# Kernel tuning notes

Hardware: AMD Instinct MI355X
Metric: run time of the kernel (lower is better)

Reference implementation:

```python
import jax, jax.numpy as jnp
import numpy as np

HID = 256
HEADS = 8
DPH = HID // HEADS  # 32
N = 65536
E = 262144


def _ln(x, g, b):
    m = jnp.mean(x, axis=-1, keepdims=True)
    v = jnp.var(x, axis=-1, keepdims=True)
    return (x - m) * jax.lax.rsqrt(v + 1e-5) * g + b


def _gelu(x):
    return jax.nn.gelu(x, approximate=False)


def _mlp2(x, W1, b1, W2, b2, act):
    return act(x @ W1 + b1) @ W2 + b2


def setup_inputs() -> dict:
    key = jax.random.key(0)
    ks = jax.random.split(key, 32)
    d = {}
    d["x"] = jax.random.normal(ks[0], (N, HID), jnp.float32)
    d["edge_index"] = jax.random.randint(ks[1], (2, E), 0, N, dtype=jnp.int32)
    d["edge_attr"] = jax.random.normal(ks[2], (E, 7), jnp.float32)
    i = 3
    def p(shape, s=0.02):
        nonlocal i
        out = jax.random.normal(ks[i], shape, jnp.float32) * s
        i += 1
        return out
    for nm, (din, dh, do) in [("q", (2 * HID + 3, 2 * HID, HID)),
                              ("k", (2 * HID + 3, 2 * HID, HID)),
                              ("v", (2 * HID + 3, 2 * HID, HID)),
                              ("s", (4, 64, HEADS)),
                              ("f", (HID, 2 * HID, HID))]:
        d[nm + "W1"] = p((din, dh))
        d[nm + "b1"] = jnp.zeros((dh,), jnp.float32)
        d[nm + "W2"] = p((dh, do))
        d[nm + "b2"] = jnp.zeros((do,), jnp.float32)
    d["ln_g"] = jnp.ones((HID,), jnp.float32)
    d["ln_b"] = jnp.zeros((HID,), jnp.float32)
    d["rW"] = p((2 * HID, HID))
    d["rb"] = jnp.zeros((HID,), jnp.float32)
    return d


def reference(x, edge_index, edge_attr,
              qW1, qb1, qW2, qb2,
              kW1, kb1, kW2, kb2,
              vW1, vb1, vW2, vb2,
              sW1, sb1, sW2, sb2,
              ln_g, ln_b, rW, rb,
              fW1, fb1, fW2, fb2):
    n_nodes = x.shape[0]
    original_x = x
    residual = x
    xn = _ln(x, ln_g, ln_b)

    src = edge_index[0]
    dst = edge_index[1]
    # gather endpoint features, concat with molecular edge feats -> [E, 2*HID+3]
    comb = jnp.concatenate([xn[src], xn[dst], edge_attr[:, :3]], axis=1)

    Q = _mlp2(comb, qW1, qb1, qW2, qb2, _gelu).reshape(-1, HEADS, DPH)
    K = _mlp2(comb, kW1, kb1, kW2, kb2, _gelu).reshape(-1, HEADS, DPH)
    V = _mlp2(comb, vW1, vb1, vW2, vb2, _gelu).reshape(-1, HEADS, DPH)

    scale = jnp.sqrt(jnp.float32(DPH))
    scores = jnp.einsum('ehd,egd->ehg', Q, K) / scale  # [E, H, H]
    bias = _mlp2(edge_attr[:, 3:7], sW1, sb1, sW2, sb2, jax.nn.relu)[:, :, None]  # [E, H, 1]
    attn = jax.nn.softmax(scores + bias, axis=1)  # softmax over dim=1, as in torch code
    wv = jnp.einsum('ehg,egd->ehd', attn, V).reshape(-1, HID)  # [E, HID]

    # scatter-mean to target nodes (edge_index[1])
    sums = jax.ops.segment_sum(wv, dst, num_segments=n_nodes)
    cnt = jax.ops.segment_sum(jnp.ones((wv.shape[0],), wv.dtype), dst, num_segments=n_nodes)
    out = sums / jnp.maximum(cnt, 1.0)[:, None]

    x1 = residual + out
    fused = jnp.concatenate([x1, original_x], axis=-1)
    x2 = x1 + (fused @ rW + rb)
    x3 = x2 + _mlp2(_ln(x2, ln_g, ln_b), fW1, fb1, fW2, fb2, _gelu)
    return x3
```

## Files before the change

### kernel.cpp

```cpp
#include <hip/hip_runtime.h>

#define N_NODES 65536
#define N_EDGES 262144
#define EBATCH 32768

typedef unsigned short u16;
typedef unsigned char u8;
typedef float f32x4 __attribute__((ext_vector_type(4)));
typedef _Float16 h2 __attribute__((ext_vector_type(2)));
typedef _Float16 v8h __attribute__((ext_vector_type(8)));

__device__ __forceinline__ u16 f2h(float f) {
  return __builtin_bit_cast(u16, (_Float16)f);
}
__device__ __forceinline__ u8 f2e5m2(float f) {
  _Float16 h = (_Float16)f;
  u16 hb = __builtin_bit_cast(u16, h);
  hb = (u16)(hb + 0x7F + ((hb >> 8) & 1));
  return (u8)(hb >> 8);
}
__device__ __forceinline__ void dec4(unsigned d, float* o) {
  o[0] = (float)__builtin_bit_cast(_Float16, (u16)((d << 8) & 0xFF00u));
  o[1] = (float)__builtin_bit_cast(_Float16, (u16)(d & 0xFF00u));
  o[2] = (float)__builtin_bit_cast(_Float16, (u16)((d >> 8) & 0xFF00u));
  o[3] = (float)__builtin_bit_cast(_Float16, (u16)((d >> 16) & 0xFF00u));
}
__device__ __forceinline__ h2 e5lo(unsigned d) {
  return __builtin_bit_cast(h2, __builtin_amdgcn_perm(d, 0u, 0x05000400u));
}
__device__ __forceinline__ h2 e5hi(unsigned d) {
  return __builtin_bit_cast(h2, __builtin_amdgcn_perm(d, 0u, 0x07000600u));
}
__device__ __forceinline__ float gelu_s(float x) {
  float e = __expf(1.702f * x);
  return x - __fdividef(x, e + 1.0f);
}
__device__ __forceinline__ float gelu_f(float x) {
  float y = 1.5957691216057308f * (x + 0.044715f * x * x * x);
  float e = __expf(y);
  return x - __fdividef(x, e + 1.0f);
}
__device__ __forceinline__ void gld16(const u16* g, u16* l) {
  __builtin_amdgcn_global_load_lds(
      (const __attribute__((address_space(1))) void*)g,
      (__attribute__((address_space(3))) void*)l, 16, 0, 0);
}

__global__ __launch_bounds__(256) void ln_kernel(const float* __restrict__ x,
                                                 const float* __restrict__ g,
                                                 const float* __restrict__ b,
                                                 u16* __restrict__ out) {
  int row = blockIdx.x * 4 + (threadIdx.x >> 6);
  int lane = threadIdx.x & 63;
  float4 v = ((const float4*)(x + (size_t)row * 256))[lane];
  float s = v.x + v.y + v.z + v.w;
  float s2 = v.x * v.x + v.y * v.y + v.z * v.z + v.w * v.w;
#pragma unroll
  for (int off = 1; off < 64; off <<= 1) {
    s += __shfl_xor(s, off, 64);
    s2 += __shfl_xor(s2, off, 64);
  }
  float mean = s * (1.0f / 256.0f);
  float var = s2 * (1.0f / 256.0f) - mean * mean;
  float rs = rsqrtf(var + 1e-5f);
  float4 gv = ((const float4*)g)[lane];
  float4 bv = ((const float4*)b)[lane];
  ushort4 o;
  o.x = f2h((v.x - mean) * rs * gv.x + bv.x);
  o.y = f2h((v.y - mean) * rs * gv.y + bv.y);
  o.z = f2h((v.z - mean) * rs * gv.z + bv.z);
  o.w = f2h((v.w - mean) * rs * gv.w + bv.w);
  *(ushort4*)(out + (size_t)row * 256 + lane * 4) = o;
}

#define GEMM_CORE(K_)                                                                   \
  const int t = threadIdx.x;                                                            \
  const int wave = t >> 6, lane = t & 63;                                               \
  const int lrow = lane & 15, quad = lane >> 4;                                         \
  const int wrow = (wave & 1) * 64, wcol = (wave >> 1) * 64;                            \
  const int sa0 = 2 * wave, sa1 = 2 * wave + 1;                                         \
  const u16* pa0 = A + (size_t)(tm + sa0 * 16 + lrow) * (K_) + quad * 8;                \
  const u16* pa1 = A + (size_t)(tm + sa1 * 16 + lrow) * (K_) + quad * 8;                \
  const u16* pb0 = BT + (size_t)(tn + sa0 * 16 + lrow) * (K_) + quad * 8;               \
  const u16* pb1 = BT + (size_t)(tn + sa1 * 16 + lrow) * (K_) + quad * 8;               \
  u16* la0 = &sAB[sa0 * 512];                                                           \
  u16* la1 = &sAB[sa1 * 512];                                                           \
  u16* lb0 = &sAB[4096 + sa0 * 512];                                                    \
  u16* lb1 = &sAB[4096 + sa1 * 512];                                                    \
  f32x4 acc[4][4];                                                                      \
  {                                                                                     \
    const f32x4 z = {0.f, 0.f, 0.f, 0.f};                                               \
    _Pragma("unroll") for (int i = 0; i < 4; ++i)                                       \
        _Pragma("unroll") for (int j = 0; j < 4; ++j) acc[i][j] = z;                    \
  }                                                                                     \
  for (int k0 = 0; k0 < (K_); k0 += 32) {                                               \
    gld16(pa0, la0);                                                                    \
    gld16(pa1, la1);                                                                    \
    gld16(pb0, lb0);                                                                    \
    gld16(pb1, lb1);                                                                    \
    pa0 += 32;                                                                          \
    pa1 += 32;                                                                          \
    pb0 += 32;                                                                          \
    pb1 += 32;                                                                          \
    __syncthreads();                                                                    \
    v8h af[4], bfv[4];                                                                  \
    _Pragma("unroll") for (int i = 0; i < 4; ++i) af[i] =                               \
        *(const v8h*)&sAB[((wave & 1) * 4 + i) * 512 + lane * 8];                       \
    _Pragma("unroll") for (int j = 0; j < 4; ++j) bfv[j] =                              \
        *(const v8h*)&sAB[4096 + ((wave >> 1) * 4 + j) * 512 + lane * 8];               \
    _Pragma("unroll") for (int i = 0; i < 4; ++i)                                       \
        _Pragma("unroll") for (int j = 0; j < 4; ++j) acc[i][j] =                       \
            __builtin_amdgcn_mfma_f32_16x16x32_f16(af[i], bfv[j], acc[i][j], 0, 0, 0);  \
    __syncthreads();                                                                    \
  }

template <typename Epi>
__global__ __launch_bounds__(256) void gemm2(const u16* __restrict__ A,
                                             const u16* __restrict__ BT,
                                             int K, int NT, Epi epi) {
  __shared__ __align__(16) u16 sAB[8192];
  const int bid = blockIdx.x;
  const int mt = bid / NT, nt = bid % NT;
  const int tm = mt * 128, tn = nt * 128;
  GEMM_CORE(K)
#pragma unroll
  for (int i = 0; i < 4; ++i)
#pragma unroll
    for (int j = 0; j < 4; ++j)
#pragma unroll
      for (int rg = 0; rg < 4; ++rg)
        epi(tm + wrow + i * 16 + quad * 4 + rg, tn + wcol + j * 16 + lrow, acc[i][j][rg]);
}

__global__ __launch_bounds__(256) void gemm2_ab(const u16* __restrict__ A,
                                                const u16* __restrict__ BT,
                                                const float* __restrict__ b1cat,
                                                u8* __restrict__ out) {
  __shared__ __align__(16) u16 sAB[8192];
  const int bid = blockIdx.x;
  const int local = bid >> 3;
  const int mt = (bid & 7) * 64 + local / 24;
  const int nt = local % 24;
  const int tm = mt * 128, tn = nt * 128;
  GEMM_CORE(256)
  float bj[4];
#pragma unroll
  for (int j = 0; j < 4; ++j)
    bj[j] = (nt < 12) ? b1cat[tn + wcol + j * 16 + lrow] : 0.f;
  u8* sb = (u8*)sAB;
#pragma unroll
  for (int i = 0; i < 4; ++i)
#pragma unroll
    for (int j = 0; j < 4; ++j)
#pragma unroll
      for (int rg = 0; rg < 4; ++rg)
        sb[(wrow + i * 16 + quad * 4 + rg) * 128 + wcol + j * 16 + lrow] =
            f2e5m2(acc[i][j][rg] + bj[j]);
  __syncthreads();
  {
    int r = t >> 1, half = t & 1;
    const uint4* sp = (const uint4*)&sb[r * 128 + half * 64];
    uint4* dp = (uint4*)(out + (size_t)(tm + r) * 3072 + tn + half * 64);
    dp[0] = sp[0];
    dp[1] = sp[1];
    dp[2] = sp[2];
    dp[3] = sp[3];
  }
}

struct EpiX2 {
  float* x2;
  const float* x1;
  const float* rb;
  __device__ void operator()(int m, int n, float v) const {
    x2[(size_t)m * 256 + n] = v + rb[n] + x1[(size_t)m * 256 + n];
  }
};
struct EpiHf {
  u16* hf;
  const float* b1;
  __device__ void operator()(int m, int n, float v) const {
    hf[(size_t)m * 512 + n] = f2h(gelu_f(v + b1[n]));
  }
};
struct EpiOut {
  float* out;
  const float* b2;
  const float* x2;
  __device__ void operator()(int m, int n, float v) const {
    out[(size_t)m * 256 + n] = v + b2[n] + x2[(size_t)m * 256 + n];
  }
};

__global__ void prep_w1catT(u16* __restrict__ out, const float* __restrict__ qW1,
                            const float* __restrict__ kW1, const float* __restrict__ vW1) {
  int cIdx = blockIdx.x;
  int rIdx = threadIdx.x;
  int sec = cIdx >> 9;
  int h = cIdx & 511;
  int mlp = sec % 3;
  const float* W1 = (mlp == 0) ? qW1 : (mlp == 1) ? kW1 : vW1;
  int rowoff = (sec < 3) ? 0 : 256;
  out[(size_t)cIdx * 256 + rIdx] = f2h(W1[(size_t)(rowoff + rIdx) * 512 + h]);
}
__global__ void prep_w2T(u16* __restrict__ out, const float* __restrict__ qW2,
                         const float* __restrict__ kW2, const float* __restrict__ vW2) {
  int row = blockIdx.x;
  int m = row >> 8, n = row & 255;
  const float* W2 = (m == 0) ? qW2 : (m == 1) ? kW2 : vW2;
  for (int k = threadIdx.x; k < 512; k += 256)
    out[(size_t)row * 512 + k] = f2h(W2[(size_t)k * 256 + n]);
}
__global__ void transpose_cast(u16* __restrict__ out, const float* __restrict__ in, int K, int Nn) {
  int n = blockIdx.x;
  for (int k = threadIdx.x; k < K; k += blockDim.x)
    out[(size_t)n * K + k] = f2h(in[(size_t)k * Nn + n]);
}
__global__ void prep_w1e16(u16* __restrict__ out, const float* __restrict__ qW1,
                           const float* __restrict__ kW1, const float* __restrict__ vW1) {
  int b = blockIdx.x;
  int m = b / 3, r = b % 3;
  const float* W1 = (m == 0) ? qW1 : (m == 1) ? kW1 : vW1;
  out[(size_t)b * 512 + threadIdx.x] = f2h(W1[(size_t)(512 + r) * 512 + threadIdx.x]);
}
__global__ void prep_b1cat(float* __restrict__ out, const float* __restrict__ qb1,
                           const float* __restrict__ kb1, const float* __restrict__ vb1) {
  int idx = blockIdx.x * 256 + threadIdx.x;
  const float* b = (idx < 512) ? qb1 : (idx < 1024) ? kb1 : vb1;
  out[idx] = b[idx & 511];
}

__global__ __launch_bounds__(256) void hist_kernel(const int* __restrict__ dst,
                                                   unsigned* __restrict__ cnt) {
  int e = blockIdx.x * 256 + threadIdx.x;
  atomicAdd(&cnt[dst[e]], 1u);
}
__global__ __launch_bounds__(1024) void scan_kernel(const unsigned* __restrict__ cnt,
                                                    unsigned* __restrict__ off,
                                                    unsigned* __restrict__ woff) {
  __shared__ unsigned s_part[1024];
  int t = threadIdx.x;
  unsigned local[64];
  unsigned run = 0;
  const uint4* cp = (const uint4*)(cnt + t * 64);
#pragma unroll
  for (int j = 0; j < 16; ++j) {
    uint4 v = cp[j];
    local[j * 4 + 0] = v.x; local[j * 4 + 1] = v.y;
    local[j * 4 + 2] = v.z; local[j * 4 + 3] = v.w;
  }
#pragma unroll
  for (int j = 0; j < 64; ++j) { unsigned c = local[j]; local[j] = run; run += c; }
  s_part[t] = run;
  __syncthreads();
  for (int d = 1; d < 1024; d <<= 1) {
    unsigned v = (t >= d) ? s_part[t - d] : 0u;
    __syncthreads();
    s_part[t] += v;
    __syncthreads();
  }
  unsigned base = (t == 0) ? 0u : s_part[t - 1];
  for (int j = 0; j < 64; ++j) {
    unsigned o = base + local[j];
    off[t * 64 + j] = o;
    woff[t * 64 + j] = o;
  }
}
__global__ __launch_bounds__(256) void scatter_ids(const int* __restrict__ dst,
                                                   unsigned* __restrict__ woff,
                                                   unsigned* __restrict__ eid) {
  int e = blockIdx.x * 256 + threadIdx.x;
  unsigned pos = atomicAdd(&woff[dst[e]], 1u);
  eid[pos] = (unsigned)e;
}

__global__ __launch_bounds__(256) void qkv_gemm(
    const int* __restrict__ eidx, const float* __restrict__ eattr,
    const u8* __restrict__ AB, const u16* __restrict__ W2T, const u16* __restrict__ w1e16,
    const float* __restrict__ qb2, const float* __restrict__ kb2, const float* __restrict__ vb2,
    int ebase, u8* __restrict__ qkv) {
  __shared__ __align__(16) u16 sH[64][136];
  __shared__ int s_src[64], s_dst[64];
  __shared__ __align__(16) float s_ea[64][4];
  const int m = blockIdx.y;
  const int t = threadIdx.x;
  const int e0 = ebase + blockIdx.x * 64;
  if (t < 64) {
    s_src[t] = eidx[e0 + t];
    s_dst[t] = eidx[N_EDGES + e0 + t];
  } else if (t >= 128 && t < 192) {
    int i = t - 128;
    const float* ea = eattr + (size_t)(e0 + i) * 7;
    s_ea[i][0] = ea[0]; s_ea[i][1] = ea[1]; s_ea[i][2] = ea[2];
  }
  __syncthreads();
  const int i = t & 63, seg = t >> 6;
  const int lane = t & 63, wave = t >> 6;
  const int lrow = lane & 15, quad = lane >> 4;
  const int wrow = (wave & 1) * 32, wcol = (wave >> 1) * 128;
  h2 ea0h, ea1h, ea2h;
  ea0h[0] = ea0h[1] = (_Float16)s_ea[i][0];
  ea1h[0] = ea1h[1] = (_Float16)s_ea[i][1];
  ea2h[0] = ea2h[1] = (_Float16)s_ea[i][2];
  const u8* rsB = AB + (size_t)s_src[i] * 3072 + m * 512 + seg * 32;
  const u8* rdB = AB + (size_t)s_dst[i] * 3072 + 1536 + m * 512 + seg * 32;
  const unsigned* w32 = (const unsigned*)(w1e16 + (size_t)m * 1536);
  f32x4 acc[2][8];
  const f32x4 z = {0.f, 0.f, 0.f, 0.f};
#pragma unroll
  for (int i2 = 0; i2 < 2; ++i2)
#pragma unroll
    for (int j = 0; j < 8; ++j) acc[i2][j] = z;
  for (int k0 = 0; k0 < 512; k0 += 128) {
    {
      alignas(16) unsigned sd[8], dd[8];
      *(uint4*)&sd[0] = *(const uint4*)(rsB + k0);
      *(uint4*)&sd[4] = *(const uint4*)(rsB + k0 + 16);
      *(uint4*)&dd[0] = *(const uint4*)(rdB + k0);
      *(uint4*)&dd[4] = *(const uint4*)(rdB + k0 + 16);
      const int cp0 = (k0 + seg * 32) >> 1;
      alignas(16) unsigned hout[16];
#pragma unroll
      for (int d = 0; d < 8; ++d) {
        int cp = cp0 + d * 2;
        h2 slo = e5lo(sd[d]) + e5lo(dd[d]);
        h2 shi = e5hi(sd[d]) + e5hi(dd[d]);
        slo += ea0h * __builtin_bit_cast(h2, w32[cp]);
        shi += ea0h * __builtin_bit_cast(h2, w32[cp + 1]);
        slo += ea1h * __builtin_bit_cast(h2, w32[256 + cp]);
        shi += ea1h * __builtin_bit_cast(h2, w32[256 + cp + 1]);
        slo += ea2h * __builtin_bit_cast(h2, w32[512 + cp]);
        shi += ea2h * __builtin_bit_cast(h2, w32[512 + cp + 1]);
        float g0 = gelu_s((float)slo[0]), g1 = gelu_s((float)slo[1]);
        float g2 = gelu_s((float)shi[0]), g3 = gelu_s((float)shi[1]);
        hout[d * 2] = (unsigned)f2h(g0) | ((unsigned)f2h(g1) << 16);
        hout[d * 2 + 1] = (unsigned)f2h(g2) | ((unsigned)f2h(g3) << 16);
      }
      uint4* hp = (uint4*)&sH[i][seg * 32];
      hp[0] = *(const uint4*)&hout[0];
      hp[1] = *(const uint4*)&hout[4];
      hp[2] = *(const uint4*)&hout[8];
      hp[3] = *(const uint4*)&hout[12];
    }
    __syncthreads();
#pragma unroll
    for (int ks = 0; ks < 4; ++ks) {
      int kk = ks * 32;
      v8h a0 = *(const v8h*)&sH[wrow + lrow][kk + quad * 8];
      v8h a1 = *(const v8h*)&sH[wrow + 16 + lrow][kk + quad * 8];
#pragma unroll
      for (int j = 0; j < 8; ++j) {
        v8h b = *(const v8h*)&W2T[(size_t)(m * 256 + wcol + j * 16 + lrow) * 512 + k0 + kk + quad * 8];
        acc[0][j] = __builtin_amdgcn_mfma_f32_16x16x32_f16(a0, b, acc[0][j], 0, 0, 0);
        acc[1][j] = __builtin_amdgcn_mfma_f32_16x16x32_f16(a1, b, acc[1][j], 0, 0, 0);
      }
    }
    __syncthreads();
  }
  const float* b2 = (m == 0) ? qb2 : (m == 1) ? kb2 : vb2;
  u8* sb = (u8*)sH;
#pragma unroll
  for (int i2 = 0; i2 < 2; ++i2)
#pragma unroll
    for (int j = 0; j < 8; ++j)
#pragma unroll
      for (int rg = 0; rg < 4; ++rg) {
        int row = wrow + i2 * 16 + quad * 4 + rg;
        int col = wcol + j * 16 + lrow;
        sb[row * 272 + col] = f2e5m2(acc[i2][j][rg] + b2[col]);
      }
  __syncthreads();
  {
    int ir = t >> 2, sg = t & 3;
    const u8* srcp = &sb[ir * 272 + sg * 64];
    uint4* dstp = (uint4*)(qkv + (size_t)(blockIdx.x * 64 + ir) * 768 + m * 256 + sg * 64);
    dstp[0] = *(const uint4*)srcp;
    dstp[1] = *(const uint4*)(srcp + 16);
    dstp[2] = *(const uint4*)(srcp + 32);
    dstp[3] = *(const uint4*)(srcp + 48);
  }
}

__global__ __launch_bounds__(256) void attn_kernel(
    const u8* __restrict__ qkv, const float* __restrict__ eattr,
    const float* __restrict__ sW1, const float* __restrict__ sb1,
    const float* __restrict__ sW2, const float* __restrict__ sb2,
    int ebase, u8* __restrict__ wv) {
  __shared__ __align__(16) u8 sQ[32][784];
  __shared__ float sS[32][8][8];
  const int t = threadIdx.x;
  const int el0 = blockIdx.x * 32;
  const int i = t >> 3, h = t & 7;
  {
    const uint4* g = (const uint4*)(qkv + (size_t)(el0 + i) * 768);
    uint4* l = (uint4*)&sQ[i][0];
#pragma unroll
    for (int j = 0; j < 6; ++j) l[h + j * 8] = g[h + j * 8];
  }
  float bias;
  {
    const float* ea = eattr + (size_t)(ebase + el0 + i) * 7;
    float a0 = ea[3], a1 = ea[4], a2 = ea[5], a3 = ea[6];
    float acc = sb2[h];
#pragma unroll 4
    for (int j = 0; j < 64; ++j) {
      float zz = fmaxf(a0 * sW1[j] + a1 * sW1[64 + j] + a2 * sW1[128 + j] + a3 * sW1[192 + j] + sb1[j], 0.f);
      acc += zz * sW2[j * 8 + h];
    }
    bias = acc;
  }
  __syncthreads();
  {
    alignas(16) unsigned qd[8];
    *(uint4*)&qd[0] = *(const uint4*)&sQ[i][h * 32];
    *(uint4*)&qd[4] = *(const uint4*)&sQ[i][h * 32 + 16];
    h2 qh[16];
#pragma unroll
    for (int d = 0; d < 8; ++d) { qh[d * 2] = e5lo(qd[d]); qh[d * 2 + 1] = e5hi(qd[d]); }
    float sc[8];
#pragma unroll
    for (int g = 0; g < 8; ++g) {
      alignas(16) unsigned kd[8];
      *(uint4*)&kd[0] = *(const uint4*)&sQ[i][256 + g * 32];
      *(uint4*)&kd[4] = *(const uint4*)&sQ[i][256 + g * 32 + 16];
      h2 acc;
      acc[0] = acc[1] = (_Float16)0.f;
#pragma unroll
      for (int d = 0; d < 8; ++d) {
        acc += qh[d * 2] * e5lo(kd[d]);
        acc += qh[d * 2 + 1] * e5hi(kd[d]);
      }
      sc[g] = (float)acc[0] + (float)acc[1];
    }
#pragma unroll
    for (int g = 0; g < 8; ++g) sS[i][h][g] = sc[g] * 0.17677669529663687f + bias;
  }
  __syncthreads();
  {
    int g = h;
    float mx = -1e30f;
#pragma unroll
    for (int hh = 0; hh < 8; ++hh) mx = fmaxf(mx, sS[i][hh][g]);
    float ev[8], ssum = 0.f;
#pragma unroll
    for (int hh = 0; hh < 8; ++hh) {
      ev[hh] = __expf(sS[i][hh][g] - mx);
      ssum += ev[hh];
    }
    float inv = 1.0f / ssum;
#pragma unroll
    for (int hh = 0; hh < 8; ++hh) sS[i][hh][g] = ev[hh] * inv;
  }
  __syncthreads();
  {
    h2 va[16];
#pragma unroll
    for (int u = 0; u < 16; ++u) va[u][0] = va[u][1] = (_Float16)0.f;
#pragma unroll
    for (int g = 0; g < 8; ++g) {
      float at = sS[i][h][g];
      h2 at2;
      at2[0] = at2[1] = (_Float16)at;
      alignas(16) unsigned vd[8];
      *(uint4*)&vd[0] = *(const uint4*)&sQ[i][512 + g * 32];
      *(uint4*)&vd[4] = *(const uint4*)&sQ[i][512 + g * 32 + 16];
#pragma unroll
      for (int d = 0; d < 8; ++d) {
        va[d * 2] += at2 * e5lo(vd[d]);
        va[d * 2 + 1] += at2 * e5hi(vd[d]);
      }
    }
    alignas(16) unsigned od[8];
#pragma unroll
    for (int p = 0; p < 8; ++p) {
      unsigned a = __builtin_bit_cast(unsigned, va[p * 2]) + 0x00800080u;
      unsigned b = __builtin_bit_cast(unsigned, va[p * 2 + 1]) + 0x00800080u;
      od[p] = __builtin_amdgcn_perm(b, a, 0x07050301u);
    }
    u8* dp = wv + (size_t)(ebase + el0 + i) * 256 + h * 32;
    *(uint4*)dp = *(const uint4*)&od[0];
    *(uint4*)(dp + 16) = *(const uint4*)&od[4];
  }
}

__global__ __launch_bounds__(256) void node_gather(const unsigned* __restrict__ off,
                                                   const unsigned* __restrict__ cnt,
                                                   const unsigned* __restrict__ eid,
                                                   const u8* __restrict__ wv,
                                                   const float* __restrict__ x,
                                                   float* __restrict__ x1,
                                                   u16* __restrict__ X1cat) {
  int n = blockIdx.x * 4 + (threadIdx.x >> 6);
  int lane = threadIdx.x & 63;
  unsigned st = off[n], c = cnt[n];
  float a0 = 0.f, a1 = 0.f, a2 = 0.f, a3 = 0.f;
  for (unsigned j = 0; j < c; ++j) {
    unsigned e = eid[st + j];
    unsigned d = *(const unsigned*)(wv + (size_t)e * 256 + lane * 4);
    float f[4];
    dec4(d, f);
    a0 += f[0]; a1 += f[1]; a2 += f[2]; a3 += f[3];
  }
  float inv = 1.0f / fmaxf((float)c, 1.0f);
  float4 xv = *(const float4*)(x + (size_t)n * 256 + lane * 4);
  float4 x1v = {xv.x + a0 * inv, xv.y + a1 * inv, xv.z + a2 * inv, xv.w + a3 * inv};
  *(float4*)(x1 + (size_t)n * 256 + lane * 4) = x1v;
  ushort4 a, bq;
  a.x = f2h(x1v.x); a.y = f2h(x1v.y); a.z = f2h(x1v.z); a.w = f2h(x1v.w);
  bq.x = f2h(xv.x); bq.y = f2h(xv.y); bq.z = f2h(xv.z); bq.w = f2h(xv.w);
  *(ushort4*)(X1cat + (size_t)n * 512 + lane * 4) = a;
  *(ushort4*)(X1cat + (size_t)n * 512 + 256 + lane * 4) = bq;
}

extern "C" void kernel_launch(void* const* d_in, const int* in_sizes, int n_in,
                              void* d_out, int out_size, void* d_ws, size_t ws_size,
                              hipStream_t stream) {
  const float* x = (const float*)d_in[0];
  const int* eidx = (const int*)d_in[1];
  const float* eattr = (const float*)d_in[2];
  const float* qW1 = (const float*)d_in[3];
  const float* qb1 = (const float*)d_in[4];
  const float* qW2 = (const float*)d_in[5];
  const float* qb2 = (const float*)d_in[6];
  const float* kW1 = (const float*)d_in[7];
  const float* kb1 = (const float*)d_in[8];
  const float* kW2 = (const float*)d_in[9];
  const float* kb2 = (const float*)d_in[10];
  const float* vW1 = (const float*)d_in[11];
  const float* vb1 = (const float*)d_in[12];
  const float* vW2 = (const float*)d_in[13];
  const float* vb2 = (const float*)d_in[14];
  const float* sW1 = (const float*)d_in[15];
  const float* sb1 = (const float*)d_in[16];
  const float* sW2 = (const float*)d_in[17];
  const float* sb2 = (const float*)d_in[18];
  const float* fW1 = (const float*)d_in[19];
  const float* fb1 = (const float*)d_in[20];
  const float* fW2 = (const float*)d_in[21];
  const float* fb2 = (const float*)d_in[22];
  const float* lng = (const float*)d_in[23];
  const float* lnb = (const float*)d_in[24];
  const float* rW = (const float*)d_in[25];
  const float* rb = (const float*)d_in[26];

  const size_t N = N_NODES;
  char* ws = (char*)d_ws;
  size_t off_b = 0;
  auto alloc = [&](size_t bytes) {
    void* p = ws + off_b;
    off_b = (off_b + bytes + 255) & ~(size_t)255;
    return p;
  };
  u16* W1catT = (u16*)alloc((size_t)3072 * 256 * 2);
  u16* W2T = (u16*)alloc((size_t)768 * 512 * 2);
  u16* rWT = (u16*)alloc((size_t)256 * 512 * 2);
  u16* fW1T = (u16*)alloc((size_t)512 * 256 * 2);
  u16* fW2T = (u16*)alloc((size_t)256 * 512 * 2);
  u16* w1e16 = (u16*)alloc((size_t)9 * 512 * 2);
  float* b1cat = (float*)alloc((size_t)1536 * 4);
  unsigned* cnt = (unsigned*)alloc(N * 4);
  unsigned* offs = (unsigned*)alloc(N * 4);
  unsigned* woff = (unsigned*)alloc(N * 4);
  unsigned* eid = (unsigned*)alloc((size_t)N_EDGES * 4);
  u8* qkv = (u8*)alloc((size_t)EBATCH * 768);
  u8* AB = (u8*)alloc(N * 3072);
  u16* xn = (u16*)d_out;
  u8* wv = (u8*)d_out;
  float* x1 = (float*)AB;
  u16* X1cat = (u16*)(AB + (size_t)67108864);
  float* x2 = (float*)(AB + (size_t)134217728);
  u16* xn2 = (u16*)AB;
  u16* Hf = (u16*)(AB + (size_t)33554432);

  hipMemsetAsync(cnt, 0, N * 4, stream);
  hist_kernel<<<N_EDGES / 256, 256, 0, stream>>>(eidx + N_EDGES, cnt);
  scan_kernel<<<1, 1024, 0, stream>>>(cnt, offs, woff);
  scatter_ids<<<N_EDGES / 256, 256, 0, stream>>>(eidx + N_EDGES, woff, eid);
  prep_w1catT<<<3072, 256, 0, stream>>>(W1catT, qW1, kW1, vW1);
  prep_w2T<<<768, 256, 0, stream>>>(W2T, qW2, kW2, vW2);
  prep_w1e16<<<9, 512, 0, stream>>>(w1e16, qW1, kW1, vW1);
  prep_b1cat<<<6, 256, 0, stream>>>(b1cat, qb1, kb1, vb1);
  transpose_cast<<<256, 256, 0, stream>>>(rWT, rW, 512, 256);
  transpose_cast<<<512, 256, 0, stream>>>(fW1T, fW1, 256, 512);
  transpose_cast<<<256, 256, 0, stream>>>(fW2T, fW2, 512, 256);

  ln_kernel<<<N_NODES / 4, 256, 0, stream>>>(x, lng, lnb, xn);
  gemm2_ab<<<12288, 256, 0, stream>>>(xn, W1catT, b1cat, AB);
  for (int b = 0; b < N_EDGES / EBATCH; ++b) {
    int ebase = b * EBATCH;
    qkv_gemm<<<dim3(EBATCH / 64, 3), 256, 0, stream>>>(eidx, eattr, AB, W2T, w1e16,
                                                       qb2, kb2, vb2, ebase, qkv);
    attn_kernel<<<EBATCH / 32, 256, 0, stream>>>(qkv, eattr, sW1, sb1, sW2, sb2, ebase, wv);
  }
  node_gather<<<N_NODES / 4, 256, 0, stream>>>(offs, cnt, eid, wv, x, x1, X1cat);
  gemm2<<<N_NODES / 128 * 2, 256, 0, stream>>>(X1cat, rWT, 512, 2, EpiX2{x2, x1, rb});
  ln_kernel<<<N_NODES / 4, 256, 0, stream>>>(x2, lng, lnb, xn2);
  gemm2<<<N_NODES / 128 * 4, 256, 0, stream>>>(xn2, fW1T, 256, 4, EpiHf{Hf, fb1});
  gemm2<<<N_NODES / 128 * 2, 256, 0, stream>>>(Hf, fW2T, 512, 2, EpiOut{(float*)d_out, fb2, x2});
}
```

Before: 1.980 ms.

## Double-buffer LDS tiles in GEMM core and pad fp8 epilogue staging

Replaces the single-buffered GEMM main loop with a double-buffered version that issues the next K-slice's global-to-LDS loads before computing on the current slice, cutting one barrier per iteration. K becomes a template parameter so the loop can fully unroll. The gemm2_ab epilogue pads its LDS staging rows to 136 bytes to reduce bank conflicts and copies out with 8-byte stores. LDS per block doubles to 32KB, which may lower occupancy.

```diff
diff --git a/kernel.cpp b/kernel.cpp
--- a/kernel.cpp
+++ b/kernel.cpp
@@ -73,56 +73,67 @@
   *(ushort4*)(out + (size_t)row * 256 + lane * 4) = o;
 }
 
-#define GEMM_CORE(K_)                                                                   \
-  const int t = threadIdx.x;                                                            \
-  const int wave = t >> 6, lane = t & 63;                                               \
-  const int lrow = lane & 15, quad = lane >> 4;                                         \
-  const int wrow = (wave & 1) * 64, wcol = (wave >> 1) * 64;                            \
-  const int sa0 = 2 * wave, sa1 = 2 * wave + 1;                                         \
-  const u16* pa0 = A + (size_t)(tm + sa0 * 16 + lrow) * (K_) + quad * 8;                \
-  const u16* pa1 = A + (size_t)(tm + sa1 * 16 + lrow) * (K_) + quad * 8;                \
-  const u16* pb0 = BT + (size_t)(tn + sa0 * 16 + lrow) * (K_) + quad * 8;               \
-  const u16* pb1 = BT + (size_t)(tn + sa1 * 16 + lrow) * (K_) + quad * 8;               \
-  u16* la0 = &sAB[sa0 * 512];                                                           \
-  u16* la1 = &sAB[sa1 * 512];                                                           \
-  u16* lb0 = &sAB[4096 + sa0 * 512];                                                    \
-  u16* lb1 = &sAB[4096 + sa1 * 512];                                                    \
-  f32x4 acc[4][4];                                                                      \
-  {                                                                                     \
-    const f32x4 z = {0.f, 0.f, 0.f, 0.f};                                               \
-    _Pragma("unroll") for (int i = 0; i < 4; ++i)                                       \
-        _Pragma("unroll") for (int j = 0; j < 4; ++j) acc[i][j] = z;                    \
-  }                                                                                     \
-  for (int k0 = 0; k0 < (K_); k0 += 32) {                                               \
-    gld16(pa0, la0);                                                                    \
-    gld16(pa1, la1);                                                                    \
-    gld16(pb0, lb0);                                                                    \
-    gld16(pb1, lb1);                                                                    \
-    pa0 += 32;                                                                          \
-    pa1 += 32;                                                                          \
-    pb0 += 32;                                                                          \
-    pb1 += 32;                                                                          \
-    __syncthreads();                                                                    \
-    v8h af[4], bfv[4];                                                                  \
-    _Pragma("unroll") for (int i = 0; i < 4; ++i) af[i] =                               \
-        *(const v8h*)&sAB[((wave & 1) * 4 + i) * 512 + lane * 8];                       \
-    _Pragma("unroll") for (int j = 0; j < 4; ++j) bfv[j] =                              \
-        *(const v8h*)&sAB[4096 + ((wave >> 1) * 4 + j) * 512 + lane * 8];               \
-    _Pragma("unroll") for (int i = 0; i < 4; ++i)                                       \
-        _Pragma("unroll") for (int j = 0; j < 4; ++j) acc[i][j] =                       \
-            __builtin_amdgcn_mfma_f32_16x16x32_f16(af[i], bfv[j], acc[i][j], 0, 0, 0);  \
-    __syncthreads();                                                                    \
-  }
-
-template <typename Epi>
+#define GEMM_DBUF(K_)                                                                    \
+  const int t = threadIdx.x;                                                             \
+  const int wave = t >> 6, lane = t & 63;                                                \
+  const int lrow = lane & 15, quad = lane >> 4;                                          \
+  const int wrow = (wave & 1) * 64, wcol = (wave >> 1) * 64;                             \
+  const int sa0 = 2 * wave, sa1 = 2 * wave + 1;                                          \
+  const u16* pa0 = A + (size_t)(tm + sa0 * 16 + lrow) * (K_) + quad * 8;                 \
+  const u16* pa1 = A + (size_t)(tm + sa1 * 16 + lrow) * (K_) + quad * 8;                 \
+  const u16* pb0 = BT + (size_t)(tn + sa0 * 16 + lrow) * (K_) + quad * 8;                \
+  const u16* pb1 = BT + (size_t)(tn + sa1 * 16 + lrow) * (K_) + quad * 8;                \
+  f32x4 acc[4][4];                                                                       \
+  {                                                                                      \
+    const f32x4 z = {0.f, 0.f, 0.f, 0.f};                                                \
+    _Pragma("unroll") for (int i = 0; i < 4; ++i)                                        \
+        _Pragma("unroll") for (int j = 0; j < 4; ++j) acc[i][j] = z;                     \
+  }                                                                                      \
+  gld16(pa0, &sAB[sa0 * 512]);                                                           \
+  gld16(pa1, &sAB[sa1 * 512]);                                                           \
+  gld16(pb0, &sAB[4096 + sa0 * 512]);                                                    \
+  gld16(pb1, &sAB[4096 + sa1 * 512]);                                                    \
+  pa0 += 32; pa1 += 32; pb0 += 32; pb1 += 32;                                            \
+  __syncthreads();                                                                       \
+  int cur = 0;                                                                           \
+  _Pragma("unroll") for (int k0 = 32; k0 < (K_); k0 += 32) {                             \
+    const int nxt = cur ^ 1;                                                             \
+    gld16(pa0, &sAB[nxt * 8192 + sa0 * 512]);                                            \
+    gld16(pa1, &sAB[nxt * 8192 + sa1 * 512]);                                            \
+    gld16(pb0, &sAB[nxt * 8192 + 4096 + sa0 * 512]);                                     \
+    gld16(pb1, &sAB[nxt * 8192 + 4096 + sa1 * 512]);                                     \
+    pa0 += 32; pa1 += 32; pb0 += 32; pb1 += 32;                                          \
+    v8h af[4], bfv[4];                                                                   \
+    _Pragma("unroll") for (int i = 0; i < 4; ++i) af[i] =                                \
+        *(const v8h*)&sAB[cur * 8192 + ((wave & 1) * 4 + i) * 512 + lane * 8];           \
+    _Pragma("unroll") for (int j = 0; j < 4; ++j) bfv[j] =                               \
+        *(const v8h*)&sAB[cur * 8192 + 4096 + ((wave >> 1) * 4 + j) * 512 + lane * 8];   \
+    _Pragma("unroll") for (int i = 0; i < 4; ++i)                                        \
+        _Pragma("unroll") for (int j = 0; j < 4; ++j) acc[i][j] =                        \
+            __builtin_amdgcn_mfma_f32_16x16x32_f16(af[i], bfv[j], acc[i][j], 0, 0, 0);   \
+    __syncthreads();                                                                     \
+    cur = nxt;                                                                           \
+  }                                                                                      \
+  {                                                                                      \
+    v8h af[4], bfv[4];                                                                   \
+    _Pragma("unroll") for (int i = 0; i < 4; ++i) af[i] =                                \
+        *(const v8h*)&sAB[cur * 8192 + ((wave & 1) * 4 + i) * 512 + lane * 8];           \
+    _Pragma("unroll") for (int j = 0; j < 4; ++j) bfv[j] =                               \
+        *(const v8h*)&sAB[cur * 8192 + 4096 + ((wave >> 1) * 4 + j) * 512 + lane * 8];   \
+    _Pragma("unroll") for (int i = 0; i < 4; ++i)                                        \
+        _Pragma("unroll") for (int j = 0; j < 4; ++j) acc[i][j] =                        \
+            __builtin_amdgcn_mfma_f32_16x16x32_f16(af[i], bfv[j], acc[i][j], 0, 0, 0);   \
+  }
+
+template <int K_, typename Epi>
 __global__ __launch_bounds__(256) void gemm2(const u16* __restrict__ A,
                                              const u16* __restrict__ BT,
-                                             int K, int NT, Epi epi) {
-  __shared__ __align__(16) u16 sAB[8192];
+                                             int NT, Epi epi) {
+  __shared__ __align__(16) u16 sAB[16384];
   const int bid = blockIdx.x;
   const int mt = bid / NT, nt = bid % NT;
   const int tm = mt * 128, tn = nt * 128;
-  GEMM_CORE(K)
+  GEMM_DBUF(K_)
 #pragma unroll
   for (int i = 0; i < 4; ++i)
 #pragma unroll
@@ -136,13 +147,14 @@
                                                 const u16* __restrict__ BT,
                                                 const float* __restrict__ b1cat,
                                                 u8* __restrict__ out) {
-  __shared__ __align__(16) u16 sAB[8192];
+  __shared__ __align__(16) u16 sAB[16384];
   const int bid = blockIdx.x;
   const int local = bid >> 3;
   const int mt = (bid & 7) * 64 + local / 24;
   const int nt = local % 24;
   const int tm = mt * 128, tn = nt * 128;
-  GEMM_CORE(256)
+  GEMM_DBUF(256)
+  __syncthreads();
   float bj[4];
 #pragma unroll
   for (int j = 0; j < 4; ++j)
@@ -154,17 +166,15 @@
     for (int j = 0; j < 4; ++j)
 #pragma unroll
       for (int rg = 0; rg < 4; ++rg)
-        sb[(wrow + i * 16 + quad * 4 + rg) * 128 + wcol + j * 16 + lrow] =
+        sb[(wrow + i * 16 + quad * 4 + rg) * 136 + wcol + j * 16 + lrow] =
             f2e5m2(acc[i][j][rg] + bj[j]);
   __syncthreads();
   {
-    int r = t >> 1, half = t & 1;
-    const uint4* sp = (const uint4*)&sb[r * 128 + half * 64];
-    uint4* dp = (uint4*)(out + (size_t)(tm + r) * 3072 + tn + half * 64);
-    dp[0] = sp[0];
-    dp[1] = sp[1];
-    dp[2] = sp[2];
-    dp[3] = sp[3];
+    int ir = t >> 1, sg = t & 1;
+    const u8* srcp = &sb[ir * 136 + sg * 64];
+    uint2* dstp = (uint2*)(out + (size_t)(tm + ir) * 3072 + tn + sg * 64);
+#pragma unroll
+    for (int q = 0; q < 8; ++q) dstp[q] = *(const uint2*)(srcp + q * 8);
   }
 }
 
@@ -593,8 +603,8 @@
     attn_kernel<<<EBATCH / 32, 256, 0, stream>>>(qkv, eattr, sW1, sb1, sW2, sb2, ebase, wv);
   }
   node_gather<<<N_NODES / 4, 256, 0, stream>>>(offs, cnt, eid, wv, x, x1, X1cat);
-  gemm2<<<N_NODES / 128 * 2, 256, 0, stream>>>(X1cat, rWT, 512, 2, EpiX2{x2, x1, rb});
+  gemm2<512><<<N_NODES / 128 * 2, 256, 0, stream>>>(X1cat, rWT, 2, EpiX2{x2, x1, rb});
   ln_kernel<<<N_NODES / 4, 256, 0, stream>>>(x2, lng, lnb, xn2);
-  gemm2<<<N_NODES / 128 * 4, 256, 0, stream>>>(xn2, fW1T, 256, 4, EpiHf{Hf, fb1});
-  gemm2<<<N_NODES / 128 * 2, 256, 0, stream>>>(Hf, fW2T, 512, 2, EpiOut{(float*)d_out, fb2, x2});
-}
+  gemm2<256><<<N_NODES / 128 * 4, 256, 0, stream>>>(xn2, fW1T, 4, EpiHf{Hf, fb1});
+  gemm2<512><<<N_NODES / 128 * 2, 256, 0, stream>>>(Hf, fW2T, 2, EpiOut{(float*)d_out, fb2, x2});
+}
```

New measurement: 2.012 ms. No clear change (+1.6%).
